# Kernel tuning notes

Hardware: AMD Instinct MI355X
Metric: run time of the kernel (lower is better)

## Reference

```python
import jax, jax.numpy as jnp
import numpy as np

B, T, D, H = 4, 2048, 1024, 16
DK = D // H

def setup_inputs() -> dict:
    key = jax.random.key(0)
    k1, k2, k3 = jax.random.split(key, 3)
    x = jax.random.normal(k1, (B, T, D), dtype=jnp.float32)
    w_qkv = jax.random.normal(k2, (D, 3 * D), dtype=jnp.float32) * (1.0 / np.sqrt(D))
    w_proj = jax.random.normal(k3, (D, D), dtype=jnp.float32) * (1.0 / np.sqrt(D))
    # additive causal mask: 0 on/below diagonal, -inf above
    neg = jnp.finfo(jnp.float32).min
    attn_mask = jnp.where(jnp.tril(jnp.ones((T, T), dtype=bool)), 0.0, neg)[None, None]
    return {"x": x, "attn_mask": attn_mask, "w_qkv": w_qkv, "w_proj": w_proj}


def reference(x, attn_mask, w_qkv, w_proj):
    Bx, Tx, Dx = x.shape
    qkv = x @ w_qkv                                  # [B,T,3D]
    q, k, v = jnp.split(qkv, 3, axis=-1)
    # [B,T,D] -> [B,H,T,dk]
    def to_heads(t):
        return t.reshape(Bx, Tx, H, DK).transpose(0, 2, 1, 3)
    q, k, v = to_heads(q), to_heads(k), to_heads(v)
    attn = jnp.einsum("bhqd,bhkd->bhqk", q, k) / jnp.sqrt(jnp.float32(DK))
    attn = attn + attn_mask
    attn = jax.nn.softmax(attn, axis=-1)
    out = jnp.einsum("bhqk,bhkd->bhqd", attn, v)     # [B,H,T,dk]
    out = out.transpose(0, 2, 1, 3).reshape(Bx, Tx, Dx)
    return out @ w_proj
```

## Files before the change

kernel.cpp:

```cpp
#include <hip/hip_runtime.h>
#include <hip/hip_bf16.h>
#include <stdint.h>

typedef __bf16 bf16x8 __attribute__((ext_vector_type(8)));
typedef __bf16 bf16x4 __attribute__((ext_vector_type(4)));
typedef float  f32x4  __attribute__((ext_vector_type(4)));

__device__ __forceinline__ void gl_lds16(const void* g, void* l) {
  __builtin_amdgcn_global_load_lds(
      (const __attribute__((address_space(1))) unsigned int*)g,
      (__attribute__((address_space(3))) unsigned int*)l, 16, 0, 0);
}

__global__ __launch_bounds__(256) void convert_x(
    const float* __restrict__ src, __bf16* __restrict__ dst) {
  const size_t i = ((size_t)blockIdx.x * 256 + threadIdx.x) * 8;
  float4 v0 = *reinterpret_cast<const float4*>(src + i);
  float4 v1 = *reinterpret_cast<const float4*>(src + i + 4);
  bf16x8 o;
  o[0] = (__bf16)v0.x; o[1] = (__bf16)v0.y; o[2] = (__bf16)v0.z; o[3] = (__bf16)v0.w;
  o[4] = (__bf16)v1.x; o[5] = (__bf16)v1.y; o[6] = (__bf16)v1.z; o[7] = (__bf16)v1.w;
  *reinterpret_cast<bf16x8*>(dst + i) = o;
}

__global__ __launch_bounds__(256) void transpose_convert(
    const float* __restrict__ src, __bf16* __restrict__ dst, int K, int N) {
  __shared__ __bf16 tile[64][65];
  const int n0 = blockIdx.x * 64, k0 = blockIdx.y * 64;
  const int t = threadIdx.x;
#pragma unroll
  for (int e = 0; e < 16; ++e) {
    int idx = e * 256 + t;
    int kk = idx >> 6, nn = idx & 63;
    tile[nn][kk] = (__bf16)src[(size_t)(k0 + kk) * N + n0 + nn];
  }
  __syncthreads();
#pragma unroll
  for (int e = 0; e < 16; ++e) {
    int idx = e * 256 + t;
    int nn = idx >> 6, kk = idx & 63;
    dst[(size_t)(n0 + nn) * K + k0 + kk] = tile[nn][kk];
  }
}

__global__ __launch_bounds__(256) void qkv_gemm(
    const __bf16* __restrict__ Xb, const __bf16* __restrict__ WT,
    __bf16* __restrict__ Qb, __bf16* __restrict__ Kb, __bf16* __restrict__ Vb) {
  __shared__ __bf16 As[128 * 32];
  __shared__ __bf16 Bs[128 * 32];
  const int t = threadIdx.x;
  const int l = t & 63, w = t >> 6;
  const int g = l >> 4, lr = l & 15;
  const int wm = w >> 1, wn = w & 1;
  const int lin = blockIdx.y * gridDim.x + blockIdx.x;
  const int cpx = (gridDim.x * gridDim.y) >> 3;
  const int swz = (lin & 7) * cpx + (lin >> 3);
  const int m0 = (swz / 24) * 128, n0 = (swz % 24) * 128;

  f32x4 acc[4][4] = {};

  for (int kb = 0; kb < 1024; kb += 32) {
#pragma unroll
    for (int rep = 0; rep < 2; ++rep) {
      int c = w * 128 + rep * 64 + l;
      int row = c >> 2, col = (c & 3) * 8;
      gl_lds16(Xb + (size_t)(m0 + row) * 1024 + kb + col,
               As + (size_t)(w * 128 + rep * 64) * 8);
      gl_lds16(WT + (size_t)(n0 + row) * 1024 + kb + col,
               Bs + (size_t)(w * 128 + rep * 64) * 8);
    }
    __syncthreads();

    bf16x8 a[4], b[4];
#pragma unroll
    for (int mf = 0; mf < 4; ++mf)
      a[mf] = *reinterpret_cast<bf16x8*>(&As[(wm * 64 + mf * 16 + lr) * 32 + g * 8]);
#pragma unroll
    for (int nf = 0; nf < 4; ++nf)
      b[nf] = *reinterpret_cast<bf16x8*>(&Bs[(wn * 64 + nf * 16 + lr) * 32 + g * 8]);
#pragma unroll
    for (int mf = 0; mf < 4; ++mf)
#pragma unroll
      for (int nf = 0; nf < 4; ++nf)
        acc[mf][nf] = __builtin_amdgcn_mfma_f32_16x16x32_bf16(
            a[mf], b[nf], acc[mf][nf], 0, 0, 0);
    __syncthreads();
  }

#pragma unroll
  for (int mf = 0; mf < 4; ++mf)
#pragma unroll
    for (int nf = 0; nf < 4; ++nf) {
      int m_ = m0 + wm * 64 + mf * 16 + g * 4;
      int n = n0 + wn * 64 + nf * 16 + lr;
      int which = n >> 10, hc = n & 1023;
      int hh = hc >> 6, dk = hc & 63;
      int bbv = m_ >> 11, tt = m_ & 2047;
      if (which == 2) {
        bf16x4 vk;
        vk[0] = (__bf16)acc[mf][nf][0]; vk[1] = (__bf16)acc[mf][nf][1];
        vk[2] = (__bf16)acc[mf][nf][2]; vk[3] = (__bf16)acc[mf][nf][3];
        *reinterpret_cast<bf16x4*>(
            &Vb[((size_t)(bbv * 16 + hh) * 64 + dk) * 2048 + tt]) = vk;
      } else {
#pragma unroll
        for (int j = 0; j < 4; ++j) {
          size_t off = (((size_t)(bbv * 16 + hh)) * 2048 + tt + j) * 64 + dk;
          float v = acc[mf][nf][j];
          if (which == 0) Qb[off] = (__bf16)(v * 0.18033688f);
          else            Kb[off] = (__bf16)v;
        }
      }
    }
}

__global__ __launch_bounds__(256) void attn_kernel(
    const __bf16* __restrict__ Qb, const __bf16* __restrict__ Kb,
    const __bf16* __restrict__ VTb, __bf16* __restrict__ Ob) {
  __shared__ __bf16 Ks[2][4096];
  __shared__ __bf16 Vs[2][4096];
  __shared__ __bf16 Pl[4][1024];
  const int t = threadIdx.x, l = t & 63, w = t >> 6;
  const int g = l >> 4, lr = l & 15;
  const int bid = blockIdx.x;
  const int logical = (bid & 7) * 128 + (bid >> 3);
  const int pi = logical & 15, bh = logical >> 4;
  const int bb = bh >> 4, h = bh & 15;
  const __bf16* Kbase = Kb  + (size_t)bh * 2048 * 64;
  const __bf16* Vbase = VTb + (size_t)bh * 64 * 2048;
  const __bf16* Qbase = Qb  + (size_t)bh * 2048 * 64;
  const int swz = (lr & 7) << 4;

  int cur = 0;
#pragma unroll 1
  for (int phase = 0; phase < 2; ++phase) {
    const int qt = phase ? (31 - pi) : pi;
    const int q0 = qt * 64;
    const int qrow = q0 + w * 16 + lr;
    const bf16x8 qf0 = *reinterpret_cast<const bf16x8*>(Qbase + (size_t)qrow * 64 + g * 8);
    const bf16x8 qf1 = *reinterpret_cast<const bf16x8*>(Qbase + (size_t)qrow * 64 + 32 + g * 8);

    f32x4 ot[4] = {};
    float lsum = 0.f;

#pragma unroll
    for (int rep = 0; rep < 2; ++rep) {
      int c = w * 128 + rep * 64 + l;
      int row = c >> 3, cc = c & 7;
      int pc = (cc ^ (row & 7)) * 8;
      gl_lds16(Kbase + (size_t)row * 64 + pc, &Ks[cur][(w * 128 + rep * 64) * 8]);
      gl_lds16(Vbase + (size_t)row * 2048 + pc, &Vs[cur][(w * 128 + rep * 64) * 8]);
    }
    __syncthreads();

    for (int kt = 0; kt <= qt; ++kt) {
      const int kv0 = kt * 64;
      if (kt < qt) {
        const int nv0 = kv0 + 64;
#pragma unroll
        for (int rep = 0; rep < 2; ++rep) {
          int c = w * 128 + rep * 64 + l;
          int row = c >> 3, cc = c & 7;
          int pc = (cc ^ (row & 7)) * 8;
          gl_lds16(Kbase + (size_t)(nv0 + row) * 64 + pc,
                   &Ks[cur ^ 1][(w * 128 + rep * 64) * 8]);
          gl_lds16(Vbase + (size_t)row * 2048 + nv0 + pc,
                   &Vs[cur ^ 1][(w * 128 + rep * 64) * 8]);
        }
      }
      f32x4 st[4];
      __builtin_amdgcn_s_setprio(1);
#pragma unroll
      for (int nf = 0; nf < 4; ++nf) {
        const char* kr = (const char*)&Ks[cur][(nf * 16 + lr) * 64];
        bf16x8 klo = *reinterpret_cast<const bf16x8*>(kr + ((g * 16) ^ swz));
        bf16x8 khi = *reinterpret_cast<const bf16x8*>(kr + (((64 + g * 16)) ^ swz));
        f32x4 z = {};
        z = __builtin_amdgcn_mfma_f32_16x16x32_bf16(klo, qf0, z, 0, 0, 0);
        st[nf] = __builtin_amdgcn_mfma_f32_16x16x32_bf16(khi, qf1, z, 0, 0, 0);
      }
      __builtin_amdgcn_s_setprio(0);
      if (kv0 == q0) {
#pragma unroll
        for (int nf = 0; nf < 4; ++nf)
#pragma unroll
          for (int j = 0; j < 4; ++j)
            if (nf * 16 + g * 4 + j > w * 16 + lr) st[nf][j] = -INFINITY;
      }
      float rs = 0.f;
#pragma unroll
      for (int nf = 0; nf < 4; ++nf)
#pragma unroll
        for (int j = 0; j < 4; ++j) {
          float p = __builtin_amdgcn_exp2f(st[nf][j]);
          st[nf][j] = p;
          rs += p;
        }
      lsum += rs;

      {
        char* prow = (char*)&Pl[w][lr * 64];
#pragma unroll
        for (int nf = 0; nf < 4; ++nf) {
          bf16x4 pk;
          pk[0] = (__bf16)st[nf][0]; pk[1] = (__bf16)st[nf][1];
          pk[2] = (__bf16)st[nf][2]; pk[3] = (__bf16)st[nf][3];
          *reinterpret_cast<bf16x4*>(prow + ((nf * 32 + g * 8) ^ swz)) = pk;
        }
      }
      {
        const char* prow = (const char*)&Pl[w][lr * 64];
        bf16x8 pb0 = *reinterpret_cast<const bf16x8*>(prow + ((g * 16) ^ swz));
        bf16x8 pb1 = *reinterpret_cast<const bf16x8*>(prow + ((64 + g * 16) ^ swz));
        __builtin_amdgcn_s_setprio(1);
#pragma unroll
        for (int nf = 0; nf < 4; ++nf) {
          const char* vr = (const char*)&Vs[cur][(nf * 16 + lr) * 64];
          bf16x8 vlo = *reinterpret_cast<const bf16x8*>(vr + ((g * 16) ^ swz));
          bf16x8 vhi = *reinterpret_cast<const bf16x8*>(vr + ((64 + g * 16) ^ swz));
          ot[nf] = __builtin_amdgcn_mfma_f32_16x16x32_bf16(vlo, pb0, ot[nf], 0, 0, 0);
          ot[nf] = __builtin_amdgcn_mfma_f32_16x16x32_bf16(vhi, pb1, ot[nf], 0, 0, 0);
        }
        __builtin_amdgcn_s_setprio(0);
      }
      __syncthreads();
      cur ^= 1;
    }

    lsum += __shfl_xor(lsum, 16);
    lsum += __shfl_xor(lsum, 32);
    const float rl = 1.f / lsum;
#pragma unroll
    for (int nf = 0; nf < 4; ++nf) {
      bf16x4 ok;
      ok[0] = (__bf16)(ot[nf][0] * rl); ok[1] = (__bf16)(ot[nf][1] * rl);
      ok[2] = (__bf16)(ot[nf][2] * rl); ok[3] = (__bf16)(ot[nf][3] * rl);
      *reinterpret_cast<bf16x4*>(
          &Ob[((size_t)(bb * 2048 + qrow)) * 1024 + h * 64 + nf * 16 + g * 4]) = ok;
    }
  }
}

__global__ __launch_bounds__(256) void proj_gemm(
    const __bf16* __restrict__ A, const __bf16* __restrict__ WT,
    float* __restrict__ Out) {
  __shared__ __bf16 As[128 * 32];
  __shared__ __bf16 Bs[128 * 32];
  const int t = threadIdx.x;
  const int l = t & 63, w = t >> 6;
  const int g = l >> 4, lr = l & 15;
  const int wm = w >> 1, wn = w & 1;
  const int lin = blockIdx.y * gridDim.x + blockIdx.x;
  const int cpx = (gridDim.x * gridDim.y) >> 3;
  const int swz = (lin & 7) * cpx + (lin >> 3);
  const int m0 = (swz >> 3) * 128, n0 = (swz & 7) * 128;

  f32x4 acc[4][4] = {};

  for (int kb = 0; kb < 1024; kb += 32) {
#pragma unroll
    for (int rep = 0; rep < 2; ++rep) {
      int c = w * 128 + rep * 64 + l;
      int row = c >> 2, col = (c & 3) * 8;
      gl_lds16(A + (size_t)(m0 + row) * 1024 + kb + col,
               As + (size_t)(w * 128 + rep * 64) * 8);
      gl_lds16(WT + (size_t)(n0 + row) * 1024 + kb + col,
               Bs + (size_t)(w * 128 + rep * 64) * 8);
    }
    __syncthreads();

    bf16x8 a[4], b[4];
#pragma unroll
    for (int mf = 0; mf < 4; ++mf)
      a[mf] = *reinterpret_cast<bf16x8*>(&As[(wm * 64 + mf * 16 + lr) * 32 + g * 8]);
#pragma unroll
    for (int nf = 0; nf < 4; ++nf)
      b[nf] = *reinterpret_cast<bf16x8*>(&Bs[(wn * 64 + nf * 16 + lr) * 32 + g * 8]);
#pragma unroll
    for (int mf = 0; mf < 4; ++mf)
#pragma unroll
      for (int nf = 0; nf < 4; ++nf)
        acc[mf][nf] = __builtin_amdgcn_mfma_f32_16x16x32_bf16(
            a[mf], b[nf], acc[mf][nf], 0, 0, 0);
    __syncthreads();
  }

#pragma unroll
  for (int mf = 0; mf < 4; ++mf)
#pragma unroll
    for (int nf = 0; nf < 4; ++nf)
#pragma unroll
      for (int j = 0; j < 4; ++j) {
        int m = m0 + wm * 64 + mf * 16 + g * 4 + j;
        int n = n0 + wn * 64 + nf * 16 + lr;
        Out[(size_t)m * 1024 + n] = acc[mf][nf][j];
      }
}

extern "C" void kernel_launch(void* const* d_in, const int* in_sizes, int n_in,
                              void* d_out, int out_size, void* d_ws, size_t ws_size,
                              hipStream_t stream) {
  const float* x      = (const float*)d_in[0];
  const float* w_qkv  = (const float*)d_in[2];
  const float* w_proj = (const float*)d_in[3];
  float* out = (float*)d_out;

  char* ws = (char*)d_ws;
  __bf16* wt_qkv  = (__bf16*)(ws);
  __bf16* wt_proj = (__bf16*)(ws + 6291456);
  __bf16* Qb      = (__bf16*)(ws + 8388608);
  __bf16* Kb      = (__bf16*)(ws + 8388608 + 16777216);
  __bf16* VTb     = (__bf16*)(ws + 8388608 + 2 * 16777216);
  __bf16* Ob      = (__bf16*)(ws + 8388608 + 3 * 16777216);
  __bf16* Xb      = Ob;

  convert_x<<<4096, 256, 0, stream>>>(x, Xb);
  transpose_convert<<<dim3(3072 / 64, 1024 / 64), 256, 0, stream>>>(w_qkv, wt_qkv, 1024, 3072);
  transpose_convert<<<dim3(1024 / 64, 1024 / 64), 256, 0, stream>>>(w_proj, wt_proj, 1024, 1024);
  qkv_gemm<<<dim3(24, 64), 256, 0, stream>>>(Xb, wt_qkv, Qb, Kb, VTb);
  attn_kernel<<<1024, 256, 0, stream>>>(Qb, Kb, VTb, Ob);
  proj_gemm<<<dim3(8, 64), 256, 0, stream>>>(Ob, wt_proj, out);
}
```

Measured before the change: 190.5 us.

## Process two adjacent query tiles per attention block to reuse K/V loads

Each attention block now handles two consecutive 64-row query tiles (128 rows) per phase instead of one, sharing each K/V tile loaded into LDS and the fragments read from it across both tiles. The grid is halved to 512 blocks, and launch bounds request two blocks per CU. This cuts global and LDS traffic per query row, at the cost of more registers, a second P buffer in LDS, and fewer blocks to balance the causal workload.

```diff
diff --git a/kernel.cpp b/kernel.cpp
--- a/kernel.cpp
+++ b/kernel.cpp
@@ -114,17 +114,18 @@
     }
 }
 
-__global__ __launch_bounds__(256) void attn_kernel(
+__global__ __launch_bounds__(256, 2) void attn_kernel(
     const __bf16* __restrict__ Qb, const __bf16* __restrict__ Kb,
     const __bf16* __restrict__ VTb, __bf16* __restrict__ Ob) {
   __shared__ __bf16 Ks[2][4096];
   __shared__ __bf16 Vs[2][4096];
-  __shared__ __bf16 Pl[4][1024];
+  __shared__ __bf16 PlA[4][1024];
+  __shared__ __bf16 PlB[4][1024];
   const int t = threadIdx.x, l = t & 63, w = t >> 6;
   const int g = l >> 4, lr = l & 15;
   const int bid = blockIdx.x;
-  const int logical = (bid & 7) * 128 + (bid >> 3);
-  const int pi = logical & 15, bh = logical >> 4;
+  const int logical = (bid & 7) * 64 + (bid >> 3);
+  const int pj = logical & 7, bh = logical >> 3;
   const int bb = bh >> 4, h = bh & 15;
   const __bf16* Kbase = Kb  + (size_t)bh * 2048 * 64;
   const __bf16* Vbase = VTb + (size_t)bh * 64 * 2048;
@@ -134,14 +135,17 @@
   int cur = 0;
 #pragma unroll 1
   for (int phase = 0; phase < 2; ++phase) {
-    const int qt = phase ? (31 - pi) : pi;
-    const int q0 = qt * 64;
-    const int qrow = q0 + w * 16 + lr;
-    const bf16x8 qf0 = *reinterpret_cast<const bf16x8*>(Qbase + (size_t)qrow * 64 + g * 8);
-    const bf16x8 qf1 = *reinterpret_cast<const bf16x8*>(Qbase + (size_t)qrow * 64 + 32 + g * 8);
-
-    f32x4 ot[4] = {};
-    float lsum = 0.f;
+    const int J = phase ? (15 - pj) : pj;
+    const int qtA = 2 * J, qtB = 2 * J + 1;
+    const int qrowA = J * 128 + w * 16 + lr;
+    const int qrowB = qrowA + 64;
+    const bf16x8 qfA0 = *reinterpret_cast<const bf16x8*>(Qbase + (size_t)qrowA * 64 + g * 8);
+    const bf16x8 qfA1 = *reinterpret_cast<const bf16x8*>(Qbase + (size_t)qrowA * 64 + 32 + g * 8);
+    const bf16x8 qfB0 = *reinterpret_cast<const bf16x8*>(Qbase + (size_t)qrowB * 64 + g * 8);
+    const bf16x8 qfB1 = *reinterpret_cast<const bf16x8*>(Qbase + (size_t)qrowB * 64 + 32 + g * 8);
+
+    f32x4 otA[4] = {}, otB[4] = {};
+    float lsA = 0.f, lsB = 0.f;
 
 #pragma unroll
     for (int rep = 0; rep < 2; ++rep) {
@@ -153,10 +157,10 @@
     }
     __syncthreads();
 
-    for (int kt = 0; kt <= qt; ++kt) {
-      const int kv0 = kt * 64;
-      if (kt < qt) {
-        const int nv0 = kv0 + 64;
+    for (int kt = 0; kt <= qtB; ++kt) {
+      const bool aAct = (kt <= qtA);
+      if (kt < qtB) {
+        const int nv0 = (kt + 1) * 64;
 #pragma unroll
         for (int rep = 0; rep < 2; ++rep) {
           int c = w * 128 + rep * 64 + l;
@@ -168,75 +172,130 @@
                    &Vs[cur ^ 1][(w * 128 + rep * 64) * 8]);
         }
       }
-      f32x4 st[4];
-      __builtin_amdgcn_s_setprio(1);
+      bf16x8 klo[4], khi[4];
 #pragma unroll
       for (int nf = 0; nf < 4; ++nf) {
         const char* kr = (const char*)&Ks[cur][(nf * 16 + lr) * 64];
-        bf16x8 klo = *reinterpret_cast<const bf16x8*>(kr + ((g * 16) ^ swz));
-        bf16x8 khi = *reinterpret_cast<const bf16x8*>(kr + (((64 + g * 16)) ^ swz));
+        klo[nf] = *reinterpret_cast<const bf16x8*>(kr + ((g * 16) ^ swz));
+        khi[nf] = *reinterpret_cast<const bf16x8*>(kr + ((64 + g * 16) ^ swz));
+      }
+      f32x4 stA[4], stB[4];
+      __builtin_amdgcn_s_setprio(1);
+#pragma unroll
+      for (int nf = 0; nf < 4; ++nf) {
         f32x4 z = {};
-        z = __builtin_amdgcn_mfma_f32_16x16x32_bf16(klo, qf0, z, 0, 0, 0);
-        st[nf] = __builtin_amdgcn_mfma_f32_16x16x32_bf16(khi, qf1, z, 0, 0, 0);
+        z = __builtin_amdgcn_mfma_f32_16x16x32_bf16(klo[nf], qfB0, z, 0, 0, 0);
+        stB[nf] = __builtin_amdgcn_mfma_f32_16x16x32_bf16(khi[nf], qfB1, z, 0, 0, 0);
+      }
+      if (aAct) {
+#pragma unroll
+        for (int nf = 0; nf < 4; ++nf) {
+          f32x4 z = {};
+          z = __builtin_amdgcn_mfma_f32_16x16x32_bf16(klo[nf], qfA0, z, 0, 0, 0);
+          stA[nf] = __builtin_amdgcn_mfma_f32_16x16x32_bf16(khi[nf], qfA1, z, 0, 0, 0);
+        }
       }
       __builtin_amdgcn_s_setprio(0);
-      if (kv0 == q0) {
+      if (kt == qtB) {
 #pragma unroll
         for (int nf = 0; nf < 4; ++nf)
 #pragma unroll
           for (int j = 0; j < 4; ++j)
-            if (nf * 16 + g * 4 + j > w * 16 + lr) st[nf][j] = -INFINITY;
-      }
-      float rs = 0.f;
-#pragma unroll
-      for (int nf = 0; nf < 4; ++nf)
-#pragma unroll
-        for (int j = 0; j < 4; ++j) {
-          float p = __builtin_amdgcn_exp2f(st[nf][j]);
-          st[nf][j] = p;
-          rs += p;
-        }
-      lsum += rs;
-
+            if (nf * 16 + g * 4 + j > w * 16 + lr) stB[nf][j] = -INFINITY;
+      }
+      if (aAct && kt == qtA) {
+#pragma unroll
+        for (int nf = 0; nf < 4; ++nf)
+#pragma unroll
+          for (int j = 0; j < 4; ++j)
+            if (nf * 16 + g * 4 + j > w * 16 + lr) stA[nf][j] = -INFINITY;
+      }
       {
-        char* prow = (char*)&Pl[w][lr * 64];
-#pragma unroll
-        for (int nf = 0; nf < 4; ++nf) {
+        float rs = 0.f;
+        char* prow = (char*)&PlB[w][lr * 64];
+#pragma unroll
+        for (int nf = 0; nf < 4; ++nf) {
+#pragma unroll
+          for (int j = 0; j < 4; ++j) {
+            float p = __builtin_amdgcn_exp2f(stB[nf][j]);
+            stB[nf][j] = p;
+            rs += p;
+          }
           bf16x4 pk;
-          pk[0] = (__bf16)st[nf][0]; pk[1] = (__bf16)st[nf][1];
-          pk[2] = (__bf16)st[nf][2]; pk[3] = (__bf16)st[nf][3];
+          pk[0] = (__bf16)stB[nf][0]; pk[1] = (__bf16)stB[nf][1];
+          pk[2] = (__bf16)stB[nf][2]; pk[3] = (__bf16)stB[nf][3];
           *reinterpret_cast<bf16x4*>(prow + ((nf * 32 + g * 8) ^ swz)) = pk;
         }
+        lsB += rs;
+      }
+      if (aAct) {
+        float rs = 0.f;
+        char* prow = (char*)&PlA[w][lr * 64];
+#pragma unroll
+        for (int nf = 0; nf < 4; ++nf) {
+#pragma unroll
+          for (int j = 0; j < 4; ++j) {
+            float p = __builtin_amdgcn_exp2f(stA[nf][j]);
+            stA[nf][j] = p;
+            rs += p;
+          }
+          bf16x4 pk;
+          pk[0] = (__bf16)stA[nf][0]; pk[1] = (__bf16)stA[nf][1];
+          pk[2] = (__bf16)stA[nf][2]; pk[3] = (__bf16)stA[nf][3];
+          *reinterpret_cast<bf16x4*>(prow + ((nf * 32 + g * 8) ^ swz)) = pk;
+        }
+        lsA += rs;
       }
       {
-        const char* prow = (const char*)&Pl[w][lr * 64];
-        bf16x8 pb0 = *reinterpret_cast<const bf16x8*>(prow + ((g * 16) ^ swz));
-        bf16x8 pb1 = *reinterpret_cast<const bf16x8*>(prow + ((64 + g * 16) ^ swz));
+        bf16x8 vlo[4], vhi[4];
+#pragma unroll
+        for (int nf = 0; nf < 4; ++nf) {
+          const char* vr = (const char*)&Vs[cur][(nf * 16 + lr) * 64];
+          vlo[nf] = *reinterpret_cast<const bf16x8*>(vr + ((g * 16) ^ swz));
+          vhi[nf] = *reinterpret_cast<const bf16x8*>(vr + ((64 + g * 16) ^ swz));
+        }
+        const char* prB = (const char*)&PlB[w][lr * 64];
+        bf16x8 pb0 = *reinterpret_cast<const bf16x8*>(prB + ((g * 16) ^ swz));
+        bf16x8 pb1 = *reinterpret_cast<const bf16x8*>(prB + ((64 + g * 16) ^ swz));
         __builtin_amdgcn_s_setprio(1);
 #pragma unroll
         for (int nf = 0; nf < 4; ++nf) {
-          const char* vr = (const char*)&Vs[cur][(nf * 16 + lr) * 64];
-          bf16x8 vlo = *reinterpret_cast<const bf16x8*>(vr + ((g * 16) ^ swz));
-          bf16x8 vhi = *reinterpret_cast<const bf16x8*>(vr + ((64 + g * 16) ^ swz));
-          ot[nf] = __builtin_amdgcn_mfma_f32_16x16x32_bf16(vlo, pb0, ot[nf], 0, 0, 0);
-          ot[nf] = __builtin_amdgcn_mfma_f32_16x16x32_bf16(vhi, pb1, ot[nf], 0, 0, 0);
+          otB[nf] = __builtin_amdgcn_mfma_f32_16x16x32_bf16(vlo[nf], pb0, otB[nf], 0, 0, 0);
+          otB[nf] = __builtin_amdgcn_mfma_f32_16x16x32_bf16(vhi[nf], pb1, otB[nf], 0, 0, 0);
         }
         __builtin_amdgcn_s_setprio(0);
+        if (aAct) {
+          const char* prA = (const char*)&PlA[w][lr * 64];
+          bf16x8 pa0 = *reinterpret_cast<const bf16x8*>(prA + ((g * 16) ^ swz));
+          bf16x8 pa1 = *reinterpret_cast<const bf16x8*>(prA + ((64 + g * 16) ^ swz));
+          __builtin_amdgcn_s_setprio(1);
+#pragma unroll
+          for (int nf = 0; nf < 4; ++nf) {
+            otA[nf] = __builtin_amdgcn_mfma_f32_16x16x32_bf16(vlo[nf], pa0, otA[nf], 0, 0, 0);
+            otA[nf] = __builtin_amdgcn_mfma_f32_16x16x32_bf16(vhi[nf], pa1, otA[nf], 0, 0, 0);
+          }
+          __builtin_amdgcn_s_setprio(0);
+        }
       }
       __syncthreads();
       cur ^= 1;
     }
 
-    lsum += __shfl_xor(lsum, 16);
-    lsum += __shfl_xor(lsum, 32);
-    const float rl = 1.f / lsum;
+    lsA += __shfl_xor(lsA, 16); lsA += __shfl_xor(lsA, 32);
+    lsB += __shfl_xor(lsB, 16); lsB += __shfl_xor(lsB, 32);
+    const float rlA = 1.f / lsA, rlB = 1.f / lsB;
 #pragma unroll
     for (int nf = 0; nf < 4; ++nf) {
       bf16x4 ok;
-      ok[0] = (__bf16)(ot[nf][0] * rl); ok[1] = (__bf16)(ot[nf][1] * rl);
-      ok[2] = (__bf16)(ot[nf][2] * rl); ok[3] = (__bf16)(ot[nf][3] * rl);
+      ok[0] = (__bf16)(otA[nf][0] * rlA); ok[1] = (__bf16)(otA[nf][1] * rlA);
+      ok[2] = (__bf16)(otA[nf][2] * rlA); ok[3] = (__bf16)(otA[nf][3] * rlA);
       *reinterpret_cast<bf16x4*>(
-          &Ob[((size_t)(bb * 2048 + qrow)) * 1024 + h * 64 + nf * 16 + g * 4]) = ok;
+          &Ob[((size_t)(bb * 2048 + qrowA)) * 1024 + h * 64 + nf * 16 + g * 4]) = ok;
+      bf16x4 ok2;
+      ok2[0] = (__bf16)(otB[nf][0] * rlB); ok2[1] = (__bf16)(otB[nf][1] * rlB);
+      ok2[2] = (__bf16)(otB[nf][2] * rlB); ok2[3] = (__bf16)(otB[nf][3] * rlB);
+      *reinterpret_cast<bf16x4*>(
+          &Ob[((size_t)(bb * 2048 + qrowB)) * 1024 + h * 64 + nf * 16 + g * 4]) = ok2;
     }
   }
 }
@@ -318,6 +377,6 @@
   transpose_convert<<<dim3(3072 / 64, 1024 / 64), 256, 0, stream>>>(w_qkv, wt_qkv, 1024, 3072);
   transpose_convert<<<dim3(1024 / 64, 1024 / 64), 256, 0, stream>>>(w_proj, wt_proj, 1024, 1024);
   qkv_gemm<<<dim3(24, 64), 256, 0, stream>>>(Xb, wt_qkv, Qb, Kb, VTb);
-  attn_kernel<<<1024, 256, 0, stream>>>(Qb, Kb, VTb, Ob);
+  attn_kernel<<<512, 256, 0, stream>>>(Qb, Kb, VTb, Ob);
   proj_gemm<<<dim3(8, 64), 256, 0, stream>>>(Ob, wt_proj, out);
 }
```

Measured after the change: 172.6 us. 1.1x faster.
